# Kernel tuning notes

Hardware: AMD Instinct MI355X
Metric: run time of the kernel (lower is better)

## Reference

```python
import jax, jax.numpy as jnp
import numpy as np

N_NODES = 100000
N_EDGES = 1200000
N_GRAPHS = 512
IN_DIM, HID, N_CLS = 16, 64, 2
EPS = 1e-5


def setup_inputs() -> dict:
    key = jax.random.key(0)
    ks = jax.random.split(key, 24)
    d = {}
    d["x"] = jax.random.normal(ks[0], (N_NODES, IN_DIM), dtype=jnp.float32)
    d["edge_index"] = jax.random.randint(ks[1], (2, N_EDGES), 0, N_NODES, dtype=jnp.int32)
    d["batch_ids"] = jnp.sort(jax.random.randint(ks[2], (N_NODES,), 0, N_GRAPHS, dtype=jnp.int32))
    # input batchnorm affine
    d["bn_in_g"] = jnp.ones((IN_DIM,), jnp.float32)
    d["bn_in_b"] = jnp.zeros((IN_DIM,), jnp.float32)
    # 3 GCN layers: weight, bias, bn gamma, bn beta
    dims = [(IN_DIM, HID), (HID, HID), (HID, HID)]
    for i, (ci, co) in enumerate(dims):
        s = 1.0 / np.sqrt(ci)
        d[f"W{i}"] = jax.random.uniform(ks[3 + 4 * i], (ci, co), jnp.float32, -s, s)
        d[f"b{i}"] = jnp.zeros((co,), jnp.float32)
        d[f"g{i}"] = jnp.ones((co,), jnp.float32)
        d[f"be{i}"] = jnp.zeros((co,), jnp.float32)
    # classifier head: Linear(HID,HID) -> ReLU -> Linear(HID,N_CLS)
    s = 1.0 / np.sqrt(HID)
    d["Wc1"] = jax.random.uniform(ks[20], (HID, HID), jnp.float32, -s, s)
    d["bc1"] = jax.random.uniform(ks[21], (HID,), jnp.float32, -s, s)
    d["Wc2"] = jax.random.uniform(ks[22], (HID, N_CLS), jnp.float32, -s, s)
    d["bc2"] = jax.random.uniform(ks[23], (N_CLS,), jnp.float32, -s, s)
    return d


def _batchnorm(x, g, b):
    # training-mode BatchNorm1d: biased batch stats over nodes
    m = jnp.mean(x, axis=0)
    v = jnp.mean(jnp.square(x - m), axis=0)
    return (x - m) * jax.lax.rsqrt(v + EPS) * g + b


def _gcn(x, W, b, src, dst, dis):
    # GCNConv: out[i] = sum_{j->i} dis[j]*dis[i] * (x_j W) + b  (self-loops included in src/dst)
    h = x @ W                                  # [N, co]
    msg = h[src] * (dis[src] * dis[dst])[:, None]  # [E+N, co] gather
    return jax.ops.segment_sum(msg, dst, num_segments=N_NODES) + b


def reference(x, bn_in_g, bn_in_b, W0, b0, g0, be0, W1, b1, g1, be1,
              W2, b2, g2, be2, Wc1, bc1, Wc2, bc2, edge_index, batch_ids):
    loops = jnp.arange(N_NODES, dtype=edge_index.dtype)
    src = jnp.concatenate([edge_index[0], loops])
    dst = jnp.concatenate([edge_index[1], loops])
    deg = jax.ops.segment_sum(jnp.ones(src.shape[0], x.dtype), dst, num_segments=N_NODES)
    dis = jnp.where(deg > 0, jax.lax.rsqrt(jnp.maximum(deg, 1e-12)), 0.0)

    h = _batchnorm(x, bn_in_g, bn_in_b)
    for W, b, g, be in ((W0, b0, g0, be0), (W1, b1, g1, be1), (W2, b2, g2, be2)):
        h = jax.nn.relu(_batchnorm(_gcn(h, W, b, src, dst, dis), g, be))

    # global mean pool over graphs
    sums = jax.ops.segment_sum(h, batch_ids, num_segments=N_GRAPHS)
    cnt = jax.ops.segment_sum(jnp.ones((N_NODES,), h.dtype), batch_ids, num_segments=N_GRAPHS)
    pooled = sums / jnp.maximum(cnt, 1.0)[:, None]

    # classifier head (dropout omitted: eval mode)
    z = jax.nn.relu(pooled @ Wc1 + bc1)
    return z @ Wc2 + bc2
```

## Files before the change

kernel.cpp:

```cpp
#include <hip/hip_runtime.h>
#include <hip/hip_bf16.h>

#define N_NODES 100000
#define N_EDGES 1200000
#define N_GRAPHS 512
#define HID 64
#define IN_DIM 16
#define EPS 1e-5f

#define NB_BUCKETS 391
#define BUCKET_SPAN 256
#define REGION 4096
#define BIN_TILE 4096
#define CSR_LEN (N_EDGES + N_NODES)
#define NREP 64

typedef _Float16 half4 __attribute__((ext_vector_type(4)));
typedef _Float16 half8 __attribute__((ext_vector_type(8)));


__global__ void bin_kernel(const int* __restrict__ ei, int* __restrict__ bucketCnt,
                           int* __restrict__ regions) {
    __shared__ int hist[NB_BUCKETS], basem[NB_BUCKETS], cur[NB_BUCKETS];
    int t = threadIdx.x;
    for (int i = t; i < NB_BUCKETS; i += 256) { hist[i] = 0; cur[i] = 0; }
    __syncthreads();
    int e0 = blockIdx.x * BIN_TILE;
    int srcs[16], dsts[16];
#pragma unroll
    for (int i = 0; i < 16; i++) {
        int e = e0 + t + i * 256;
        if (e < N_EDGES) {
            srcs[i] = ei[e];
            dsts[i] = ei[N_EDGES + e];
            atomicAdd(&hist[dsts[i] >> 8], 1);
        } else {
            dsts[i] = -1;
        }
    }
    __syncthreads();
    for (int i = t; i < NB_BUCKETS; i += 256) {
        int h = hist[i];
        basem[i] = h ? atomicAdd(&bucketCnt[i], h) : 0;
    }
    __syncthreads();
#pragma unroll
    for (int i = 0; i < 16; i++) {
        if (dsts[i] >= 0) {
            int b = dsts[i] >> 8;
            int pos = basem[b] + atomicAdd(&cur[b], 1);
            if (pos < REGION)
                regions[b * REGION + pos] = srcs[i] | ((dsts[i] & 255) << 17);
        }
    }
}

__global__ void build_kernel(const int* __restrict__ regions, const int* __restrict__ bucketCnt,
                             int* __restrict__ csrOff, int* __restrict__ csrSrc,
                             float* __restrict__ dis) {
    __shared__ int deg[256], off[256], cur[256];
    __shared__ int slice[REGION + 256];
    __shared__ int sTot, sBase;
    int b = blockIdx.x, t = threadIdx.x;
    {
        int s = 0;
        for (int i = t; i < NB_BUCKETS; i += 256)
            if (i < b) s += min(bucketCnt[i], REGION);
        deg[t] = s;
        __syncthreads();
        for (int k = 128; k > 0; k >>= 1) {
            if (t < k) deg[t] += deg[t + k];
            __syncthreads();
        }
        if (t == 0) sBase = deg[0] + b * BUCKET_SPAN;
        __syncthreads();
    }
    int bb = sBase;
    int cnt = min(bucketCnt[b], REGION);
    int nbase = b * BUCKET_SPAN;
    int n = nbase + t;
    bool valid = (n < N_NODES);
    deg[t] = valid ? 1 : 0;
    __syncthreads();
    for (int i = t; i < cnt; i += 256) {
        int rec = regions[b * REGION + i];
        atomicAdd(&deg[rec >> 17], 1);
    }
    __syncthreads();
    int d = deg[t];
    off[t] = d;
    __syncthreads();
    for (int s = 1; s < 256; s <<= 1) {
        int v = (t >= s) ? off[t - s] : 0;
        __syncthreads();
        off[t] += v;
        __syncthreads();
    }
    int excl = off[t] - d;
    if (valid) {
        csrOff[n] = bb + excl;
        dis[n] = rsqrtf((float)d);
    }
    if (b == 0 && t == 0) csrOff[N_NODES] = CSR_LEN;
    if (t == 255) sTot = off[255];
    cur[t] = excl;
    __syncthreads();
    if (valid) {
        int pos = atomicAdd(&cur[t], 1);
        slice[pos] = n;
    }
    for (int i = t; i < cnt; i += 256) {
        int rec = regions[b * REGION + i];
        int pos = atomicAdd(&cur[rec >> 17], 1);
        slice[pos] = rec & 0x1FFFF;
    }
    __syncthreads();
    int tot = sTot;
    for (int i = t; i < tot; i += 256) csrSrc[bb + i] = slice[i];
}


__global__ void stats_x(const float* __restrict__ x, float* __restrict__ sums,
                        float* __restrict__ sumsq, _Float16* __restrict__ hwBuf) {
    __shared__ float ls[16], lq[16];
    int t = threadIdx.x;
    if (blockIdx.x == 0 && t < 8)
        ((float4*)(hwBuf + (size_t)N_NODES * HID))[t] = make_float4(0.f, 0.f, 0.f, 0.f);
    if (t < 16) { ls[t] = 0.f; lq[t] = 0.f; }
    __syncthreads();
    float s = 0.f, q = 0.f;
    const int total = N_NODES * IN_DIM;
    for (int i = blockIdx.x * blockDim.x + t; i < total; i += gridDim.x * blockDim.x) {
        float v = x[i];
        s += v; q += v * v;
    }
    int k = t & 15;
    atomicAdd(&ls[k], s);
    atomicAdd(&lq[k], q);
    __syncthreads();
    if (t < 16) { atomicAdd(&sums[t], ls[t]); atomicAdd(&sumsq[t], lq[t]); }
}

__device__ __forceinline__ void bn_coef(const float* sums, const float* sumsq,
                                        const float* gamma, const float* beta, int k,
                                        float& sc, float& sh) {
    const float invn = 1.0f / (float)N_NODES;
    float m = sums[k] * invn;
    float var = sumsq[k] * invn - m * m;
    float rs = rsqrtf(var + EPS);
    sc = gamma[k] * rs;
    sh = beta[k] - m * sc;
}

__global__ void reduce_stats(const float* __restrict__ rep, float* __restrict__ outStats) {
    int j = threadIdx.x;
    float s = 0.f;
    for (int r = 0; r < NREP; r++) s += rep[r * 128 + j];
    outStats[j] = s;
}


__global__ void premsg_kernel(const float* __restrict__ x, const float* __restrict__ sums,
                              const float* __restrict__ sumsq, const float* __restrict__ gamma,
                              const float* __restrict__ beta, const float* __restrict__ dis,
                              half4* __restrict__ m4) {
    __shared__ float sc16[16], sh16[16];
    int t = threadIdx.x;
    if (t < 16) bn_coef(sums, sumsq, gamma, beta, t, sc16[t], sh16[t]);
    __syncthreads();
    int idx = blockIdx.x * 256 + t;
    if (idx < (N_NODES + 1) * 4) {
        int n = idx >> 2, c = idx & 3;
        half4 o;
        o.x = (_Float16)0.f; o.y = (_Float16)0.f; o.z = (_Float16)0.f; o.w = (_Float16)0.f;
        if (n < N_NODES) {
            float4 h = ((const float4*)x)[idx];
            float d = dis[n];
            o.x = (_Float16)((h.x * sc16[c * 4 + 0] + sh16[c * 4 + 0]) * d);
            o.y = (_Float16)((h.y * sc16[c * 4 + 1] + sh16[c * 4 + 1]) * d);
            o.z = (_Float16)((h.z * sc16[c * 4 + 2] + sh16[c * 4 + 2]) * d);
            o.w = (_Float16)((h.w * sc16[c * 4 + 3] + sh16[c * 4 + 3]) * d);
        }
        m4[idx] = o;
    }
}

__global__ void agg16_gemm0_kernel(const half4* __restrict__ m4, const int* __restrict__ csrOff,
                                   const int* __restrict__ csrSrc, const float* __restrict__ dis,
                                   const float* __restrict__ W, const float* __restrict__ bias,
                                   float* __restrict__ y, float* __restrict__ statsRep) {
    const int t = threadIdx.x;
    const int lane = t & 63;
    const int wid = t >> 6;
    const int g = lane >> 4;
    const int s = lane & 15;
    const int fl = s & 3;
    const int q = s >> 2;
    const int wave = blockIdx.x * 4 + wid;
    const int nwaves = gridDim.x * 4;

    float wreg[16][4];
#pragma unroll
    for (int k = 0; k < 16; k++) {
#pragma unroll
        for (int j = 0; j < 4; j++) wreg[k][j] = W[k * HID + s + 16 * j];
    }
    float bj[4];
#pragma unroll
    for (int j = 0; j < 4; j++) bj[j] = bias[s + 16 * j];
    float sv[4] = {0.f, 0.f, 0.f, 0.f}, qv[4] = {0.f, 0.f, 0.f, 0.f};

    for (int n0 = wave * 4; n0 < N_NODES; n0 += nwaves * 4) {
        int n = n0 + g;
        bool vn = (n < N_NODES);
        int beg = 0, end = 0;
        if (vn) { beg = csrOff[n]; end = csrOff[n + 1]; }
        float4 acc = make_float4(0.f, 0.f, 0.f, 0.f);
        int e = beg + q;
        int i0 = (e < end) ? csrSrc[e] : N_NODES;
        int i1 = (e + 4 < end) ? csrSrc[e + 4] : N_NODES;
        while (e < end) {
            int j0 = i0, j1 = i1;
            e += 8;
            i0 = (e < end) ? csrSrc[e] : N_NODES;
            i1 = (e + 4 < end) ? csrSrc[e + 4] : N_NODES;
            half4 v0 = m4[(size_t)j0 * 4 + fl];
            half4 v1 = m4[(size_t)j1 * 4 + fl];
            acc.x += (float)v0.x + (float)v1.x;
            acc.y += (float)v0.y + (float)v1.y;
            acc.z += (float)v0.z + (float)v1.z;
            acc.w += (float)v0.w + (float)v1.w;
        }
        acc.x += __shfl_xor(acc.x, 4, 64);  acc.y += __shfl_xor(acc.y, 4, 64);
        acc.z += __shfl_xor(acc.z, 4, 64);  acc.w += __shfl_xor(acc.w, 4, 64);
        acc.x += __shfl_xor(acc.x, 8, 64);  acc.y += __shfl_xor(acc.y, 8, 64);
        acc.z += __shfl_xor(acc.z, 8, 64);  acc.w += __shfl_xor(acc.w, 8, 64);
        float d = vn ? dis[n] : 0.f;
        acc.x *= d; acc.y *= d; acc.z *= d; acc.w *= d;
        float yv0 = bj[0], yv1 = bj[1], yv2 = bj[2], yv3 = bj[3];
        const int gbase = lane & 48;
#pragma unroll
        for (int k = 0; k < 16; k++) {
            float comp = ((k & 3) == 0) ? acc.x : ((k & 3) == 1) ? acc.y
                        : ((k & 3) == 2) ? acc.z : acc.w;
            float a = __shfl(comp, gbase + (k >> 2), 64);
            yv0 += a * wreg[k][0];
            yv1 += a * wreg[k][1];
            yv2 += a * wreg[k][2];
            yv3 += a * wreg[k][3];
        }
        if (vn) {
            float* yr = y + (size_t)n * HID;
            yr[s] = yv0; yr[s + 16] = yv1; yr[s + 32] = yv2; yr[s + 48] = yv3;
            sv[0] += yv0; qv[0] += yv0 * yv0;
            sv[1] += yv1; qv[1] += yv1 * yv1;
            sv[2] += yv2; qv[2] += yv2 * yv2;
            sv[3] += yv3; qv[3] += yv3 * yv3;
        }
    }
#pragma unroll
    for (int j = 0; j < 4; j++) {
        sv[j] += __shfl_xor(sv[j], 16, 64); sv[j] += __shfl_xor(sv[j], 32, 64);
        qv[j] += __shfl_xor(qv[j], 16, 64); qv[j] += __shfl_xor(qv[j], 32, 64);
    }
    __shared__ float ls[4][64], lq[4][64];
    if (g == 0) {
#pragma unroll
        for (int j = 0; j < 4; j++) { ls[wid][s + 16 * j] = sv[j]; lq[wid][s + 16 * j] = qv[j]; }
    }
    __syncthreads();
    if (wid == 0) {
        float S = ls[0][lane] + ls[1][lane] + ls[2][lane] + ls[3][lane];
        float Q = lq[0][lane] + lq[1][lane] + lq[2][lane] + lq[3][lane];
        float* rep = statsRep + (blockIdx.x & (NREP - 1)) * 128;
        atomicAdd(&rep[lane], S);
        atomicAdd(&rep[64 + lane], Q);
    }
}


#define G64_ROWS 128
__global__ void gemm64_kernel(const float* __restrict__ hin, const float* __restrict__ W,
                              const float* __restrict__ sums, const float* __restrict__ sumsq,
                              const float* __restrict__ gamma, const float* __restrict__ beta,
                              const float* __restrict__ dis, _Float16* __restrict__ hout) {
    __shared__ float Ws[HID * HID];
    __shared__ float hs[G64_ROWS][HID + 1];
    __shared__ float scb[64], shb[64];
    int t = threadIdx.x;
    int fg = t & 15;
    int rg = t >> 4;
    int base = blockIdx.x * G64_ROWS;

    if (t < 64) bn_coef(sums, sumsq, gamma, beta, t, scb[t], shb[t]);
    {
        const float4* W4 = (const float4*)W;
        float4* Ws4 = (float4*)Ws;
        for (int i = t; i < HID * HID / 4; i += 256) Ws4[i] = W4[i];
    }
    __syncthreads();
    {
        const float4* hin4 = (const float4*)hin;
        for (int i = t; i < G64_ROWS * 16; i += 256) {
            int r = i >> 4, c = i & 15;
            int n = base + r;
            float4 v = make_float4(0.f, 0.f, 0.f, 0.f);
            if (n < N_NODES) {
                float4 h = hin4[n * 16 + c];
                v.x = fmaxf(h.x * scb[c * 4 + 0] + shb[c * 4 + 0], 0.f);
                v.y = fmaxf(h.y * scb[c * 4 + 1] + shb[c * 4 + 1], 0.f);
                v.z = fmaxf(h.z * scb[c * 4 + 2] + shb[c * 4 + 2], 0.f);
                v.w = fmaxf(h.w * scb[c * 4 + 3] + shb[c * 4 + 3], 0.f);
            }
            hs[r][c * 4 + 0] = v.x;
            hs[r][c * 4 + 1] = v.y;
            hs[r][c * 4 + 2] = v.z;
            hs[r][c * 4 + 3] = v.w;
        }
    }
    __syncthreads();

    float4 acc[8];
#pragma unroll
    for (int r = 0; r < 8; r++) acc[r] = make_float4(0.f, 0.f, 0.f, 0.f);
    const float4* Ws4 = (const float4*)Ws;
    for (int k = 0; k < HID; k++) {
        float4 wk = Ws4[k * 16 + fg];
#pragma unroll
        for (int r = 0; r < 8; r++) {
            float h = hs[rg * 8 + r][k];
            acc[r].x += h * wk.x;
            acc[r].y += h * wk.y;
            acc[r].z += h * wk.z;
            acc[r].w += h * wk.w;
        }
    }
    half4* hout4 = (half4*)hout;
#pragma unroll
    for (int r = 0; r < 8; r++) {
        int n = base + rg * 8 + r;
        if (n < N_NODES) {
            float dsc = dis[n];
            half4 o;
            o.x = (_Float16)(acc[r].x * dsc);
            o.y = (_Float16)(acc[r].y * dsc);
            o.z = (_Float16)(acc[r].z * dsc);
            o.w = (_Float16)(acc[r].w * dsc);
            hout4[n * 16 + fg] = o;
        }
    }
}


__global__ void aggregate_kernel(const half8* __restrict__ hwh, const int* __restrict__ csrOff,
                                 const int* __restrict__ csrSrc, const float* __restrict__ dis,
                                 const float* __restrict__ bias, float4* __restrict__ y4,
                                 float* __restrict__ statsRep) {
    const int lane = threadIdx.x & 63;
    const int wid = threadIdx.x >> 6;
    const int g = lane >> 5;
    const int s = lane & 31;
    const int c = s & 7;
    const int o = s >> 3;
    const int wave = blockIdx.x * 4 + wid;
    const int nwaves = gridDim.x * 4;

    const float4 bv0 = ((const float4*)bias)[c * 2];
    const float4 bv1 = ((const float4*)bias)[c * 2 + 1];
    float sa[8], qa[8];
#pragma unroll
    for (int j = 0; j < 8; j++) { sa[j] = 0.f; qa[j] = 0.f; }

    for (int n0 = wave * 2; n0 < N_NODES; n0 += nwaves * 2) {
        int n = n0 + g;
        bool vn = (n < N_NODES);
        int beg = 0, end = 0;
        if (vn) { beg = csrOff[n]; end = csrOff[n + 1]; }
        float acc[8];
#pragma unroll
        for (int j = 0; j < 8; j++) acc[j] = 0.f;
        int e = beg + o;
        int i0 = (e < end) ? csrSrc[e] : N_NODES;
        int i1 = (e + 4 < end) ? csrSrc[e + 4] : N_NODES;
        while (e < end) {
            int j0 = i0, j1 = i1;
            e += 8;
            i0 = (e < end) ? csrSrc[e] : N_NODES;
            i1 = (e + 4 < end) ? csrSrc[e + 4] : N_NODES;
            half8 h0 = hwh[(size_t)j0 * 8 + c];
            half8 h1 = hwh[(size_t)j1 * 8 + c];
#pragma unroll
            for (int j = 0; j < 8; j++) acc[j] += (float)h0[j] + (float)h1[j];
        }
#pragma unroll
        for (int j = 0; j < 8; j++) {
            acc[j] += __shfl_xor(acc[j], 8, 64);
            acc[j] += __shfl_xor(acc[j], 16, 64);
        }
        if (o == 0 && vn) {
            float d = dis[n];
            float val[8];
            val[0] = acc[0] * d + bv0.x; val[1] = acc[1] * d + bv0.y;
            val[2] = acc[2] * d + bv0.z; val[3] = acc[3] * d + bv0.w;
            val[4] = acc[4] * d + bv1.x; val[5] = acc[5] * d + bv1.y;
            val[6] = acc[6] * d + bv1.z; val[7] = acc[7] * d + bv1.w;
            y4[(size_t)n * 16 + c * 2] = make_float4(val[0], val[1], val[2], val[3]);
            y4[(size_t)n * 16 + c * 2 + 1] = make_float4(val[4], val[5], val[6], val[7]);
#pragma unroll
            for (int j = 0; j < 8; j++) { sa[j] += val[j]; qa[j] += val[j] * val[j]; }
        }
    }
#pragma unroll
    for (int j = 0; j < 8; j++) {
        sa[j] += __shfl_xor(sa[j], 32, 64);
        qa[j] += __shfl_xor(qa[j], 32, 64);
    }
    __shared__ float ls[4][64], lq[4][64];
    ls[wid][lane] = 0.f;
    lq[wid][lane] = 0.f;
    if (lane < 8) {
#pragma unroll
        for (int j = 0; j < 8; j++) { ls[wid][lane * 8 + j] = sa[j]; lq[wid][lane * 8 + j] = qa[j]; }
    }
    __syncthreads();
    if (wid == 0) {
        float S = ls[0][lane] + ls[1][lane] + ls[2][lane] + ls[3][lane];
        float Q = lq[0][lane] + lq[1][lane] + lq[2][lane] + lq[3][lane];
        float* rep = statsRep + (blockIdx.x & (NREP - 1)) * 128;
        atomicAdd(&rep[lane], S);
        atomicAdd(&rep[64 + lane], Q);
    }
}


#define POOL_CHUNK 256
__global__ void pool_kernel(const float* __restrict__ y, const int* __restrict__ batch,
                            const float* __restrict__ sums, const float* __restrict__ sumsq,
                            const float* __restrict__ gamma, const float* __restrict__ beta,
                            float* __restrict__ pool, float* __restrict__ cnt) {
    int f = threadIdx.x & 63;
    int nl = threadIdx.x >> 6;
    float sc, sh;
    bn_coef(sums, sumsq, gamma, beta, f, sc, sh);
    int base = blockIdx.x * POOL_CHUNK;
    int endn = min(base + POOL_CHUNK, N_NODES);
    int g_cur = -1;
    float acc = 0.f;
    float c_acc = 0.f;
    for (int n = base + nl; n < endn; n += 4) {
        int g = batch[n];
        float v = fmaxf(y[n * HID + f] * sc + sh, 0.f);
        if (g != g_cur) {
            if (g_cur >= 0) {
                atomicAdd(&pool[g_cur * HID + f], acc);
                if (f == 0) atomicAdd(&cnt[g_cur], c_acc);
            }
            g_cur = g;
            acc = 0.f;
            c_acc = 0.f;
        }
        acc += v;
        c_acc += 1.f;
    }
    if (g_cur >= 0) {
        atomicAdd(&pool[g_cur * HID + f], acc);
        if (f == 0) atomicAdd(&cnt[g_cur], c_acc);
    }
}

__global__ void head_kernel(const float* __restrict__ pool, const float* __restrict__ cnt,
                            const float* __restrict__ Wc1, const float* __restrict__ bc1,
                            const float* __restrict__ Wc2, const float* __restrict__ bc2,
                            float* __restrict__ out) {
    int g = blockIdx.x;
    int f = threadIdx.x;
    __shared__ float p[64], z[64];
    float c = fmaxf(cnt[g], 1.0f);
    p[f] = pool[g * HID + f] / c;
    __syncthreads();
    float acc = bc1[f];
    for (int k = 0; k < 64; k++) acc += p[k] * Wc1[k * 64 + f];
    z[f] = fmaxf(acc, 0.f);
    __syncthreads();
    if (f < 2) {
        float o = bc2[f];
        for (int k = 0; k < 64; k++) o += z[k] * Wc2[k * 2 + f];
        out[g * 2 + f] = o;
    }
}


extern "C" void kernel_launch(void* const* d_in, const int* in_sizes, int n_in,
                              void* d_out, int out_size, void* d_ws, size_t ws_size,
                              hipStream_t stream) {
    const float* x      = (const float*)d_in[0];
    const int*   ei     = (const int*)d_in[1];
    const int*   batch  = (const int*)d_in[2];
    const float* bn_in_g = (const float*)d_in[3];
    const float* bn_in_b = (const float*)d_in[4];
    const float* W0 = (const float*)d_in[5];
    const float* b0 = (const float*)d_in[6];
    const float* g0 = (const float*)d_in[7];
    const float* be0 = (const float*)d_in[8];
    const float* W1 = (const float*)d_in[9];
    const float* b1 = (const float*)d_in[10];
    const float* g1 = (const float*)d_in[11];
    const float* be1 = (const float*)d_in[12];
    const float* W2 = (const float*)d_in[13];
    const float* b2 = (const float*)d_in[14];
    const float* g2 = (const float*)d_in[15];
    const float* be2 = (const float*)d_in[16];
    const float* Wc1 = (const float*)d_in[17];
    const float* bc1 = (const float*)d_in[18];
    const float* Wc2 = (const float*)d_in[19];
    const float* bc2 = (const float*)d_in[20];
    float* out = (float*)d_out;

    char* w = (char*)d_ws;
    size_t off = 0;
    auto take = [&](size_t bytes) {
        size_t r = off;
        off += (bytes + 255) & ~(size_t)255;
        return r;
    };
    float* stats    = (float*)(w + take(4 * 256 * 4));
    float* statsRep = (float*)(w + take(3 * NREP * 128 * 4));
    float* pool     = (float*)(w + take((size_t)N_GRAPHS * HID * 4));
    float* cnt      = (float*)(w + take((size_t)N_GRAPHS * 4));
    int* bucketCnt  = (int*)(w + take((size_t)NB_BUCKETS * 4));
    size_t zero_end = off;
    float* dis    = (float*)(w + take((size_t)N_NODES * 4));
    int* csrOff   = (int*)(w + take((size_t)(N_NODES + 1) * 4));
    int* csrSrc   = (int*)(w + take((size_t)(CSR_LEN + 64) * 4));
    _Float16* hwBuf = (_Float16*)(w + take((size_t)(N_NODES + 1) * HID * 2));
    float* yBuf   = (float*)(w + take((size_t)N_NODES * HID * 4));
    _Float16* msgBuf = (_Float16*)(w + take((size_t)(N_NODES + 1) * IN_DIM * 2));
    int* regions  = (int*)hwBuf;
    (void)ws_size; (void)n_in; (void)in_sizes; (void)out_size;

    hipMemsetAsync(w, 0, zero_end, stream);

    const int nbBin   = (N_EDGES + BIN_TILE - 1) / BIN_TILE;
    const int nbPre   = ((N_NODES + 1) * 4 + 255) / 256;
    const int nbG64   = (N_NODES + G64_ROWS - 1) / G64_ROWS;
    const int nbAgg16 = (N_NODES + 16 * 4 - 1) / (16 * 4);
    const int nbAgg64 = (N_NODES + 8 * 4 - 1) / (8 * 4);

    bin_kernel<<<nbBin, 256, 0, stream>>>(ei, bucketCnt, regions);
    build_kernel<<<NB_BUCKETS, 256, 0, stream>>>(regions, bucketCnt, csrOff, csrSrc, dis);

    float* s0 = stats + 0 * 256;
    float* s1 = stats + 1 * 256;
    float* s2 = stats + 2 * 256;
    float* s3 = stats + 3 * 256;
    float* rep1 = statsRep + 0 * NREP * 128;
    float* rep2 = statsRep + 1 * NREP * 128;
    float* rep3 = statsRep + 2 * NREP * 128;

    stats_x<<<256, 256, 0, stream>>>(x, s0, s0 + 64, hwBuf);

    premsg_kernel<<<nbPre, 256, 0, stream>>>(x, s0, s0 + 64, bn_in_g, bn_in_b, dis,
                                             (half4*)msgBuf);
    agg16_gemm0_kernel<<<nbAgg16, 256, 0, stream>>>((const half4*)msgBuf, csrOff, csrSrc, dis,
                                                    W0, b0, yBuf, rep1);
    reduce_stats<<<1, 128, 0, stream>>>(rep1, s1);

    gemm64_kernel<<<nbG64, 256, 0, stream>>>(yBuf, W1, s1, s1 + 64, g0, be0, dis, hwBuf);
    aggregate_kernel<<<nbAgg64, 256, 0, stream>>>((const half8*)hwBuf, csrOff, csrSrc, dis, b1,
                                                  (float4*)yBuf, rep2);
    reduce_stats<<<1, 128, 0, stream>>>(rep2, s2);

    gemm64_kernel<<<nbG64, 256, 0, stream>>>(yBuf, W2, s2, s2 + 64, g1, be1, dis, hwBuf);
    aggregate_kernel<<<nbAgg64, 256, 0, stream>>>((const half8*)hwBuf, csrOff, csrSrc, dis, b2,
                                                  (float4*)yBuf, rep3);
    reduce_stats<<<1, 128, 0, stream>>>(rep3, s3);

    const int nbPool = (N_NODES + POOL_CHUNK - 1) / POOL_CHUNK;
    pool_kernel<<<nbPool, 256, 0, stream>>>(yBuf, batch, s3, s3 + 64, g2, be2, pool, cnt);
    head_kernel<<<N_GRAPHS, 64, 0, stream>>>(pool, cnt, Wc1, bc1, Wc2, bc2, out);
}
```

Baseline: 320.0 us.

## Store intermediate activations in fp16, fold stat reduction into consumers, vectorize edge loads

Pre-BN activations in yBuf now go out as fp16 instead of fp32, which halves the bytes written by the aggregation kernels and read by the GEMM and pool kernels. The three single-block reduce_stats launches are removed, and each consumer block now sums the NREP replicated partial stats itself when it computes its BN coefficients. bin_kernel loads edges as int4, and the gemm64 inner loop is unrolled by two using float2 shared-memory reads. The risks are lost precision from fp16 storage of unnormalized values and redundant stat reduction in every block.

```diff
diff --git a/kernel.cpp b/kernel.cpp
--- a/kernel.cpp
+++ b/kernel.cpp
@@ -25,17 +25,26 @@
     int t = threadIdx.x;
     for (int i = t; i < NB_BUCKETS; i += 256) { hist[i] = 0; cur[i] = 0; }
     __syncthreads();
-    int e0 = blockIdx.x * BIN_TILE;
+    const int4* ei4s = (const int4*)ei;
+    const int4* ei4d = (const int4*)(ei + N_EDGES);
     int srcs[16], dsts[16];
 #pragma unroll
-    for (int i = 0; i < 16; i++) {
-        int e = e0 + t + i * 256;
-        if (e < N_EDGES) {
-            srcs[i] = ei[e];
-            dsts[i] = ei[N_EDGES + e];
-            atomicAdd(&hist[dsts[i] >> 8], 1);
+    for (int i = 0; i < 4; i++) {
+        int idx4 = blockIdx.x * (BIN_TILE / 4) + t + i * 256;
+        if (idx4 * 4 < N_EDGES) {
+            int4 s4 = ei4s[idx4];
+            int4 d4 = ei4d[idx4];
+            srcs[i * 4 + 0] = s4.x; dsts[i * 4 + 0] = d4.x;
+            srcs[i * 4 + 1] = s4.y; dsts[i * 4 + 1] = d4.y;
+            srcs[i * 4 + 2] = s4.z; dsts[i * 4 + 2] = d4.z;
+            srcs[i * 4 + 3] = s4.w; dsts[i * 4 + 3] = d4.w;
+            atomicAdd(&hist[d4.x >> 8], 1);
+            atomicAdd(&hist[d4.y >> 8], 1);
+            atomicAdd(&hist[d4.z >> 8], 1);
+            atomicAdd(&hist[d4.w >> 8], 1);
         } else {
-            dsts[i] = -1;
+            dsts[i * 4 + 0] = -1; dsts[i * 4 + 1] = -1;
+            dsts[i * 4 + 2] = -1; dsts[i * 4 + 3] = -1;
         }
     }
     __syncthreads();
@@ -152,11 +161,16 @@
     sh = beta[k] - m * sc;
 }
 
-__global__ void reduce_stats(const float* __restrict__ rep, float* __restrict__ outStats) {
-    int j = threadIdx.x;
-    float s = 0.f;
-    for (int r = 0; r < NREP; r++) s += rep[r * 128 + j];
-    outStats[j] = s;
+__device__ __forceinline__ void bn_coef_rep(const float* rep, const float* gamma,
+                                            const float* beta, int k, float& sc, float& sh) {
+    float S = 0.f, Q = 0.f;
+    for (int r = 0; r < NREP; r++) { S += rep[r * 128 + k]; Q += rep[r * 128 + 64 + k]; }
+    const float invn = 1.0f / (float)N_NODES;
+    float m = S * invn;
+    float var = Q * invn - m * m;
+    float rs = rsqrtf(var + EPS);
+    sc = gamma[k] * rs;
+    sh = beta[k] - m * sc;
 }
 
 
@@ -188,7 +202,7 @@
 __global__ void agg16_gemm0_kernel(const half4* __restrict__ m4, const int* __restrict__ csrOff,
                                    const int* __restrict__ csrSrc, const float* __restrict__ dis,
                                    const float* __restrict__ W, const float* __restrict__ bias,
-                                   float* __restrict__ y, float* __restrict__ statsRep) {
+                                   _Float16* __restrict__ y, float* __restrict__ statsRep) {
     const int t = threadIdx.x;
     const int lane = t & 63;
     const int wid = t >> 6;
@@ -250,8 +264,9 @@
             yv3 += a * wreg[k][3];
         }
         if (vn) {
-            float* yr = y + (size_t)n * HID;
-            yr[s] = yv0; yr[s + 16] = yv1; yr[s + 32] = yv2; yr[s + 48] = yv3;
+            _Float16* yr = y + (size_t)n * HID;
+            yr[s] = (_Float16)yv0; yr[s + 16] = (_Float16)yv1;
+            yr[s + 32] = (_Float16)yv2; yr[s + 48] = (_Float16)yv3;
             sv[0] += yv0; qv[0] += yv0 * yv0;
             sv[1] += yv1; qv[1] += yv1 * yv1;
             sv[2] += yv2; qv[2] += yv2 * yv2;
@@ -280,19 +295,19 @@
 
 
 #define G64_ROWS 128
-__global__ void gemm64_kernel(const float* __restrict__ hin, const float* __restrict__ W,
-                              const float* __restrict__ sums, const float* __restrict__ sumsq,
-                              const float* __restrict__ gamma, const float* __restrict__ beta,
-                              const float* __restrict__ dis, _Float16* __restrict__ hout) {
+__global__ void gemm64_kernel(const _Float16* __restrict__ hin, const float* __restrict__ W,
+                              const float* __restrict__ statsRep, const float* __restrict__ gamma,
+                              const float* __restrict__ beta, const float* __restrict__ dis,
+                              _Float16* __restrict__ hout) {
     __shared__ float Ws[HID * HID];
-    __shared__ float hs[G64_ROWS][HID + 1];
+    __shared__ float hs[G64_ROWS][HID + 2];
     __shared__ float scb[64], shb[64];
     int t = threadIdx.x;
     int fg = t & 15;
     int rg = t >> 4;
     int base = blockIdx.x * G64_ROWS;
 
-    if (t < 64) bn_coef(sums, sumsq, gamma, beta, t, scb[t], shb[t]);
+    if (t < 64) bn_coef_rep(statsRep, gamma, beta, t, scb[t], shb[t]);
     {
         const float4* W4 = (const float4*)W;
         float4* Ws4 = (float4*)Ws;
@@ -300,17 +315,17 @@
     }
     __syncthreads();
     {
-        const float4* hin4 = (const float4*)hin;
+        const half4* hin4 = (const half4*)hin;
         for (int i = t; i < G64_ROWS * 16; i += 256) {
             int r = i >> 4, c = i & 15;
             int n = base + r;
             float4 v = make_float4(0.f, 0.f, 0.f, 0.f);
             if (n < N_NODES) {
-                float4 h = hin4[n * 16 + c];
-                v.x = fmaxf(h.x * scb[c * 4 + 0] + shb[c * 4 + 0], 0.f);
-                v.y = fmaxf(h.y * scb[c * 4 + 1] + shb[c * 4 + 1], 0.f);
-                v.z = fmaxf(h.z * scb[c * 4 + 2] + shb[c * 4 + 2], 0.f);
-                v.w = fmaxf(h.w * scb[c * 4 + 3] + shb[c * 4 + 3], 0.f);
+                half4 h = hin4[n * 16 + c];
+                v.x = fmaxf((float)h.x * scb[c * 4 + 0] + shb[c * 4 + 0], 0.f);
+                v.y = fmaxf((float)h.y * scb[c * 4 + 1] + shb[c * 4 + 1], 0.f);
+                v.z = fmaxf((float)h.z * scb[c * 4 + 2] + shb[c * 4 + 2], 0.f);
+                v.w = fmaxf((float)h.w * scb[c * 4 + 3] + shb[c * 4 + 3], 0.f);
             }
             hs[r][c * 4 + 0] = v.x;
             hs[r][c * 4 + 1] = v.y;
@@ -324,15 +339,16 @@
 #pragma unroll
     for (int r = 0; r < 8; r++) acc[r] = make_float4(0.f, 0.f, 0.f, 0.f);
     const float4* Ws4 = (const float4*)Ws;
-    for (int k = 0; k < HID; k++) {
-        float4 wk = Ws4[k * 16 + fg];
+    for (int k = 0; k < HID; k += 2) {
+        float4 wk0 = Ws4[k * 16 + fg];
+        float4 wk1 = Ws4[(k + 1) * 16 + fg];
 #pragma unroll
         for (int r = 0; r < 8; r++) {
-            float h = hs[rg * 8 + r][k];
-            acc[r].x += h * wk.x;
-            acc[r].y += h * wk.y;
-            acc[r].z += h * wk.z;
-            acc[r].w += h * wk.w;
+            float2 h2 = *(const float2*)&hs[rg * 8 + r][k];
+            acc[r].x += h2.x * wk0.x + h2.y * wk1.x;
+            acc[r].y += h2.x * wk0.y + h2.y * wk1.y;
+            acc[r].z += h2.x * wk0.z + h2.y * wk1.z;
+            acc[r].w += h2.x * wk0.w + h2.y * wk1.w;
         }
     }
     half4* hout4 = (half4*)hout;
@@ -354,7 +370,7 @@
 
 __global__ void aggregate_kernel(const half8* __restrict__ hwh, const int* __restrict__ csrOff,
                                  const int* __restrict__ csrSrc, const float* __restrict__ dis,
-                                 const float* __restrict__ bias, float4* __restrict__ y4,
+                                 const float* __restrict__ bias, half8* __restrict__ y8,
                                  float* __restrict__ statsRep) {
     const int lane = threadIdx.x & 63;
     const int wid = threadIdx.x >> 6;
@@ -404,8 +420,10 @@
             val[2] = acc[2] * d + bv0.z; val[3] = acc[3] * d + bv0.w;
             val[4] = acc[4] * d + bv1.x; val[5] = acc[5] * d + bv1.y;
             val[6] = acc[6] * d + bv1.z; val[7] = acc[7] * d + bv1.w;
-            y4[(size_t)n * 16 + c * 2] = make_float4(val[0], val[1], val[2], val[3]);
-            y4[(size_t)n * 16 + c * 2 + 1] = make_float4(val[4], val[5], val[6], val[7]);
+            half8 ov;
+#pragma unroll
+            for (int j = 0; j < 8; j++) ov[j] = (_Float16)val[j];
+            y8[(size_t)n * 8 + c] = ov;
 #pragma unroll
             for (int j = 0; j < 8; j++) { sa[j] += val[j]; qa[j] += val[j] * val[j]; }
         }
@@ -434,14 +452,17 @@
 
 
 #define POOL_CHUNK 256
-__global__ void pool_kernel(const float* __restrict__ y, const int* __restrict__ batch,
-                            const float* __restrict__ sums, const float* __restrict__ sumsq,
-                            const float* __restrict__ gamma, const float* __restrict__ beta,
-                            float* __restrict__ pool, float* __restrict__ cnt) {
-    int f = threadIdx.x & 63;
-    int nl = threadIdx.x >> 6;
-    float sc, sh;
-    bn_coef(sums, sumsq, gamma, beta, f, sc, sh);
+__global__ void pool_kernel(const _Float16* __restrict__ y, const int* __restrict__ batch,
+                            const float* __restrict__ statsRep, const float* __restrict__ gamma,
+                            const float* __restrict__ beta, float* __restrict__ pool,
+                            float* __restrict__ cnt) {
+    __shared__ float scs[64], shs[64];
+    int t = threadIdx.x;
+    int f = t & 63;
+    int nl = t >> 6;
+    if (t < 64) bn_coef_rep(statsRep, gamma, beta, t, scs[t], shs[t]);
+    __syncthreads();
+    float sc = scs[f], sh = shs[f];
     int base = blockIdx.x * POOL_CHUNK;
     int endn = min(base + POOL_CHUNK, N_NODES);
     int g_cur = -1;
@@ -449,7 +470,7 @@
     float c_acc = 0.f;
     for (int n = base + nl; n < endn; n += 4) {
         int g = batch[n];
-        float v = fmaxf(y[n * HID + f] * sc + sh, 0.f);
+        float v = fmaxf((float)y[(size_t)n * HID + f] * sc + sh, 0.f);
         if (g != g_cur) {
             if (g_cur >= 0) {
                 atomicAdd(&pool[g_cur * HID + f], acc);
@@ -523,7 +544,7 @@
         off += (bytes + 255) & ~(size_t)255;
         return r;
     };
-    float* stats    = (float*)(w + take(4 * 256 * 4));
+    float* stats    = (float*)(w + take(256 * 4));
     float* statsRep = (float*)(w + take(3 * NREP * 128 * 4));
     float* pool     = (float*)(w + take((size_t)N_GRAPHS * HID * 4));
     float* cnt      = (float*)(w + take((size_t)N_GRAPHS * 4));
@@ -533,7 +554,7 @@
     int* csrOff   = (int*)(w + take((size_t)(N_NODES + 1) * 4));
     int* csrSrc   = (int*)(w + take((size_t)(CSR_LEN + 64) * 4));
     _Float16* hwBuf = (_Float16*)(w + take((size_t)(N_NODES + 1) * HID * 2));
-    float* yBuf   = (float*)(w + take((size_t)N_NODES * HID * 4));
+    _Float16* yBuf  = (_Float16*)(w + take((size_t)N_NODES * HID * 2));
     _Float16* msgBuf = (_Float16*)(w + take((size_t)(N_NODES + 1) * IN_DIM * 2));
     int* regions  = (int*)hwBuf;
     (void)ws_size; (void)n_in; (void)in_sizes; (void)out_size;
@@ -549,10 +570,7 @@
     bin_kernel<<<nbBin, 256, 0, stream>>>(ei, bucketCnt, regions);
     build_kernel<<<NB_BUCKETS, 256, 0, stream>>>(regions, bucketCnt, csrOff, csrSrc, dis);
 
-    float* s0 = stats + 0 * 256;
-    float* s1 = stats + 1 * 256;
-    float* s2 = stats + 2 * 256;
-    float* s3 = stats + 3 * 256;
+    float* s0 = stats;
     float* rep1 = statsRep + 0 * NREP * 128;
     float* rep2 = statsRep + 1 * NREP * 128;
     float* rep3 = statsRep + 2 * NREP * 128;
@@ -563,19 +581,15 @@
                                              (half4*)msgBuf);
     agg16_gemm0_kernel<<<nbAgg16, 256, 0, stream>>>((const half4*)msgBuf, csrOff, csrSrc, dis,
                                                     W0, b0, yBuf, rep1);
-    reduce_stats<<<1, 128, 0, stream>>>(rep1, s1);
-
-    gemm64_kernel<<<nbG64, 256, 0, stream>>>(yBuf, W1, s1, s1 + 64, g0, be0, dis, hwBuf);
+
+    gemm64_kernel<<<nbG64, 256, 0, stream>>>(yBuf, W1, rep1, g0, be0, dis, hwBuf);
     aggregate_kernel<<<nbAgg64, 256, 0, stream>>>((const half8*)hwBuf, csrOff, csrSrc, dis, b1,
-                                                  (float4*)yBuf, rep2);
-    reduce_stats<<<1, 128, 0, stream>>>(rep2, s2);
-
-    gemm64_kernel<<<nbG64, 256, 0, stream>>>(yBuf, W2, s2, s2 + 64, g1, be1, dis, hwBuf);
+                                                  (half8*)yBuf, rep2);
+    gemm64_kernel<<<nbG64, 256, 0, stream>>>(yBuf, W2, rep2, g1, be1, dis, hwBuf);
     aggregate_kernel<<<nbAgg64, 256, 0, stream>>>((const half8*)hwBuf, csrOff, csrSrc, dis, b2,
-                                                  (float4*)yBuf, rep3);
-    reduce_stats<<<1, 128, 0, stream>>>(rep3, s3);
+                                                  (half8*)yBuf, rep3);
 
     const int nbPool = (N_NODES + POOL_CHUNK - 1) / POOL_CHUNK;
-    pool_kernel<<<nbPool, 256, 0, stream>>>(yBuf, batch, s3, s3 + 64, g2, be2, pool, cnt);
+    pool_kernel<<<nbPool, 256, 0, stream>>>(yBuf, batch, rep3, g2, be2, pool, cnt);
     head_kernel<<<N_GRAPHS, 64, 0, stream>>>(pool, cnt, Wc1, bc1, Wc2, bc2, out);
 }
```

New measurement: 311.7 us. 1.03x faster.
